# Performance work log

Hardware: AMD Instinct MI355X
Metric: run time of the kernel (lower is better)

Reference implementation:

```python
import jax, jax.numpy as jnp
import numpy as np

NUM_EXPERTS = 8


def setup_inputs() -> dict:
    key = jax.random.key(0)
    k1, k2, k3, k4 = jax.random.split(key, 4)
    T, H, I, E = 1024, 1024, 4096, NUM_EXPERTS
    return {
        "hidden_states": jax.random.normal(k1, (T, H), dtype=jnp.float32),
        "w1": jax.random.normal(k2, (E, 2 * I, H), dtype=jnp.float32) * 0.02,
        "w2": jax.random.normal(k3, (E, H, I), dtype=jnp.float32) * 0.02,
        "gating_output": jax.random.normal(k4, (T, E), dtype=jnp.float32),
        "topk": 2,
    }


def reference(hidden_states, w1, w2, gating_output, topk):
    # Faithful single-device version of jax_fused_moe_func (renormalize=True,
    # reduce_results=True). The original sorts token copies by expert id and runs
    # a grouped matmul (megablox gmm), then reverts the sort; mathematically each
    # token copy is multiplied by its expert's weights, which we compute directly
    # (no sort/unsort permutation needed since it cancels).
    orig_shape = hidden_states.shape
    dtype = hidden_states.dtype
    H = hidden_states.shape[-1]
    T = hidden_states.size // H
    E = w1.shape[0]
    I = w2.shape[-1]  # intermediate_size

    hs = hidden_states.reshape(T, H)
    gates = gating_output.reshape(T, E)

    probs = jax.nn.softmax(gates.astype(jnp.float32), axis=-1)
    topk_weights, topk_indices = jax.lax.top_k(probs, k=topk)
    topk_weights = topk_weights / topk_weights.sum(axis=-1, keepdims=True)  # renormalize
    topk_weights = topk_weights.astype(dtype)

    flat_ids = topk_indices.reshape(-1)            # [T*topk] expert id per token copy
    x = jnp.repeat(hs, topk, axis=0)               # [T*topk, H] token copies

    out = jnp.zeros((T * topk, H), dtype=dtype)
    for e in range(E):  # fixed small expert loop (emulates grouped GEMM)
        h = x @ w1[e].T                            # [m, 2I]
        act = jax.nn.silu(h[:, :I]) * h[:, I:]     # SwiGLU
        y = act @ w2[e].T                          # [m, H]
        out = jnp.where((flat_ids == e)[:, None], y, out)

    out = (out.reshape(T, topk, H) * topk_weights[..., None]).sum(axis=-2)
    return out.reshape(orig_shape)
```

## Files before the change

kernel.cpp:

```cpp
#include <hip/hip_runtime.h>

#define T_TOK 1024
#define H_DIM 1024
#define I_DIM 4096
#define NE 8

typedef __attribute__((ext_vector_type(8))) short bf16x8;
typedef __attribute__((ext_vector_type(4))) float f32x4;
typedef __attribute__((ext_vector_type(8))) unsigned short us8;

__device__ __forceinline__ unsigned short f2bf(float x) {
  union { float f; unsigned u; } v; v.f = x;
  unsigned r = v.u + 0x7fffu + ((v.u >> 16) & 1u);
  return (unsigned short)(r >> 16);
}

__device__ __forceinline__ unsigned cvt_pk_bf16(float a, float b) {
  unsigned r;
  asm("v_cvt_pk_bf16_f32 %0, %1, %2" : "=v"(r) : "v"(a), "v"(b));
  return r;
}

__device__ __forceinline__ void sync_lds() {
  asm volatile("s_waitcnt lgkmcnt(0)" ::: "memory");
  __builtin_amdgcn_s_barrier();
}

__global__ void k_route(const float* __restrict__ gates, int* __restrict__ counts,
                        int* __restrict__ tok_idx, float* __restrict__ tok_w,
                        int* __restrict__ tok_cpy) {
  int t = blockIdx.x * blockDim.x + threadIdx.x;
  if (t >= T_TOK) return;
  float g[NE];
#pragma unroll
  for (int e = 0; e < NE; ++e) g[e] = gates[t * NE + e];
  int i1 = 0; float g1 = g[0];
#pragma unroll
  for (int e = 1; e < NE; ++e) if (g[e] > g1) { g1 = g[e]; i1 = e; }
  int i2 = -1; float g2 = -1e30f;
#pragma unroll
  for (int e = 0; e < NE; ++e) if (e != i1 && g[e] > g2) { g2 = g[e]; i2 = e; }
  float wa = 1.0f / (1.0f + expf(g2 - g1));
  float wb = 1.0f - wa;
  int s1 = atomicAdd(&counts[i1], 1);
  tok_idx[i1 * T_TOK + s1] = t; tok_w[i1 * T_TOK + s1] = wa; tok_cpy[i1 * T_TOK + s1] = 0;
  int s2 = atomicAdd(&counts[i2], 1);
  tok_idx[i2 * T_TOK + s2] = t; tok_w[i2 * T_TOK + s2] = wb; tok_cpy[i2 * T_TOK + s2] = 1;
}

__global__ void k_pack(const float* __restrict__ hs, const int* __restrict__ counts,
                       const int* __restrict__ tok_idx, const float* __restrict__ tok_w,
                       const int* __restrict__ tok_cpy, unsigned short* __restrict__ xpack,
                       float* __restrict__ row_w, int* __restrict__ inv_row) {
  int e = blockIdx.x >> 10, slot = blockIdx.x & 1023;
  if (slot >= counts[e]) return;
  int off = 0;
#pragma unroll
  for (int i = 0; i < NE; ++i) if (i < e) off += counts[i];
  int row = off + slot;
  int tok = tok_idx[e * T_TOK + slot];
  if (threadIdx.x == 0) {
    row_w[row] = tok_w[e * T_TOK + slot];
    inv_row[tok * 2 + tok_cpy[e * T_TOK + slot]] = row;
  }
  float4 v = ((const float4*)(hs + (size_t)tok * H_DIM))[threadIdx.x];
  uint2 o; o.x = cvt_pk_bf16(v.x, v.y); o.y = cvt_pk_bf16(v.z, v.w);
  ((uint2*)(xpack + (size_t)row * H_DIM))[threadIdx.x] = o;
}

#define BK 64

__global__ __launch_bounds__(256)
void k_gemm1(const float* __restrict__ w1, const unsigned short* __restrict__ xpack,
             const int* __restrict__ counts, unsigned short* __restrict__ act) {
  int b = blockIdx.x;
  int panel = b & 1023;
  int mt = b >> 10;
  int e = panel >> 7, ntile = panel & 127;
  int cnt = counts[e];
  int m0 = mt * 128;
  if (m0 >= cnt) return;
  int off = 0;
#pragma unroll
  for (int i = 0; i < NE; ++i) if (i < e) off += counts[i];
  int n0 = ntile * 32;

  __shared__ __align__(16) short As[2][128 * BK];
  __shared__ __align__(16) short Bs[2][64 * BK];

  int tid = threadIdx.x;
  int lane = tid & 63, wid = tid >> 6;
  int wm = wid & 1, wn = wid >> 1;
  int lr = lane & 15, lk8 = (lane >> 4) * 8;

  const float* w1e = w1 + (size_t)e * (2 * I_DIM) * H_DIM;
  const unsigned short* xb = xpack + (size_t)(off + m0) * H_DIM;

  int arow0 = tid >> 3, ack = tid & 7;
  int brow0 = tid >> 4, bck = tid & 15;

  const unsigned short* aptr[4];
  int awoff[4];
#pragma unroll
  for (int i = 0; i < 4; ++i) {
    int r = arow0 + i * 32;
    aptr[i] = xb + (size_t)r * H_DIM + ack * 8;
    awoff[i] = r * BK + ((ack * 8) ^ ((r & 7) << 3));
  }
  const float* bptr[4];
  int bwoff[4];
#pragma unroll
  for (int i = 0; i < 4; ++i) {
    int r = brow0 + i * 16;
    int grow = ((r & 16) ? I_DIM : 0) + n0 + ((r >> 5) << 4) + (r & 15);
    bptr[i] = w1e + (size_t)grow * H_DIM + bck * 4;
    bwoff[i] = r * BK + ((bck * 4) ^ ((r & 7) << 3));
  }

  f32x4 acc[4][2];
#pragma unroll
  for (int i = 0; i < 4; ++i)
#pragma unroll
    for (int j = 0; j < 2; ++j) acc[i][j] = (f32x4){0.f, 0.f, 0.f, 0.f};

  us8 aReg[2][4];
  float4 bReg[2][4];

#define G1_LOAD(SET, KSTEP)                                                     \
  {                                                                             \
    int kq = (KSTEP)*BK;                                                        \
    _Pragma("unroll") for (int i = 0; i < 4; ++i) {                             \
      us8 z = {0, 0, 0, 0, 0, 0, 0, 0};                                         \
      aReg[SET][i] = (m0 + arow0 + i * 32 < cnt) ? *(const us8*)(aptr[i] + kq) : z; \
    }                                                                           \
    _Pragma("unroll") for (int i = 0; i < 4; ++i)                               \
        bReg[SET][i] = *(const float4*)(bptr[i] + kq);                          \
  }

#define G1_STEP(BUF, SET, NEXTK)                                                \
  {                                                                             \
    _Pragma("unroll") for (int i = 0; i < 4; ++i)                               \
        *(us8*)&As[BUF][awoff[i]] = aReg[SET][i];                               \
    _Pragma("unroll") for (int i = 0; i < 4; ++i) {                             \
      float4 v = bReg[SET][i];                                                  \
      uint2 o; o.x = cvt_pk_bf16(v.x, v.y); o.y = cvt_pk_bf16(v.z, v.w);        \
      *(uint2*)&Bs[BUF][bwoff[i]] = o;                                          \
    }                                                                           \
    if ((NEXTK) < H_DIM / BK) G1_LOAD(SET, NEXTK);                              \
    sync_lds();                                                                 \
    _Pragma("unroll") for (int kk = 0; kk < 2; ++kk) {                          \
      int k0 = kk * 32 + lk8;                                                   \
      bf16x8 a[4], bb[2];                                                       \
      _Pragma("unroll") for (int mr = 0; mr < 4; ++mr) {                        \
        int r = wm * 64 + mr * 16 + lr;                                         \
        a[mr] = *(const bf16x8*)&As[BUF][r * BK + (k0 ^ ((r & 7) << 3))];       \
      }                                                                         \
      _Pragma("unroll") for (int nr = 0; nr < 2; ++nr) {                        \
        int r = (wn * 2 + nr) * 16 + lr;                                        \
        bb[nr] = *(const bf16x8*)&Bs[BUF][r * BK + (k0 ^ ((r & 7) << 3))];      \
      }                                                                         \
      _Pragma("unroll") for (int mr = 0; mr < 4; ++mr)                          \
          _Pragma("unroll") for (int nr = 0; nr < 2; ++nr)                      \
              acc[mr][nr] = __builtin_amdgcn_mfma_f32_16x16x32_bf16(            \
                  a[mr], bb[nr], acc[mr][nr], 0, 0, 0);                         \
    }                                                                           \
  }

  G1_LOAD(0, 0);
  G1_LOAD(1, 1);
  for (int ks = 0; ks < H_DIM / BK; ks += 2) {
    G1_STEP(0, 0, ks + 2);
    G1_STEP(1, 1, ks + 3);
  }
#undef G1_LOAD
#undef G1_STEP

#pragma unroll
  for (int mr = 0; mr < 4; ++mr) {
    f32x4 g = acc[mr][0], u = acc[mr][1];
    int ncol = n0 + wn * 16 + lr;
#pragma unroll
    for (int q = 0; q < 4; ++q) {
      int rl = wm * 64 + mr * 16 + (lane >> 4) * 4 + q;
      if (m0 + rl < cnt) {
        float gv = g[q];
        float av = gv / (1.0f + expf(-gv)) * u[q];
        act[(size_t)(off + m0 + rl) * I_DIM + ncol] = f2bf(av);
      }
    }
  }
}

__global__ __launch_bounds__(256)
void k_gemm2(const float* __restrict__ w2, const unsigned short* __restrict__ act,
             const int* __restrict__ counts, const float* __restrict__ row_w,
             float* __restrict__ yp) {
  int b = blockIdx.x;
  int panel = b & 511;
  int mt = b >> 9;
  int e = panel >> 6;
  int nt = (panel & 63) >> 2, kc = panel & 3;
  int cnt = counts[e];
  int m0 = mt * 64;
  if (m0 >= cnt) return;
  int off = 0;
#pragma unroll
  for (int i = 0; i < NE; ++i) if (i < e) off += counts[i];
  int n0 = nt * 64;
  int kbase = kc * 1024;

  __shared__ __align__(16) short As[2][64 * BK];
  __shared__ __align__(16) short Bs[2][64 * BK];

  int tid = threadIdx.x;
  int lane = tid & 63, wid = tid >> 6;
  int wm = wid & 1, wn = wid >> 1;
  int lr = lane & 15, lk8 = (lane >> 4) * 8;

  const float* w2e = w2 + (size_t)e * H_DIM * I_DIM;
  const unsigned short* ab = act + (size_t)(off + m0) * I_DIM;

  int arow0 = tid >> 3, ack = tid & 7;
  int brow0 = tid >> 4, bck = tid & 15;

  const unsigned short* aptr[2];
  int awoff[2];
#pragma unroll
  for (int i = 0; i < 2; ++i) {
    int r = arow0 + i * 32;
    aptr[i] = ab + (size_t)r * I_DIM + kbase + ack * 8;
    awoff[i] = r * BK + ((ack * 8) ^ ((r & 7) << 3));
  }
  const float* bptr[4];
  int bwoff[4];
#pragma unroll
  for (int i = 0; i < 4; ++i) {
    int r = brow0 + i * 16;
    bptr[i] = w2e + (size_t)(n0 + r) * I_DIM + kbase + bck * 4;
    bwoff[i] = r * BK + ((bck * 4) ^ ((r & 7) << 3));
  }

  f32x4 acc[2][2];
#pragma unroll
  for (int i = 0; i < 2; ++i)
#pragma unroll
    for (int j = 0; j < 2; ++j) acc[i][j] = (f32x4){0.f, 0.f, 0.f, 0.f};

  us8 aReg[2][2];
  float4 bReg[2][4];

#define G2_LOAD(SET, KSTEP)                                                     \
  {                                                                             \
    int kq = (KSTEP)*BK;                                                        \
    _Pragma("unroll") for (int i = 0; i < 2; ++i) {                             \
      us8 z = {0, 0, 0, 0, 0, 0, 0, 0};                                         \
      aReg[SET][i] = (m0 + arow0 + i * 32 < cnt) ? *(const us8*)(aptr[i] + kq) : z; \
    }                                                                           \
    _Pragma("unroll") for (int i = 0; i < 4; ++i)                               \
        bReg[SET][i] = *(const float4*)(bptr[i] + kq);                          \
  }

#define G2_STEP(BUF, SET, NEXTK)                                                \
  {                                                                             \
    _Pragma("unroll") for (int i = 0; i < 2; ++i)                               \
        *(us8*)&As[BUF][awoff[i]] = aReg[SET][i];                               \
    _Pragma("unroll") for (int i = 0; i < 4; ++i) {                             \
      float4 v = bReg[SET][i];                                                  \
      uint2 o; o.x = cvt_pk_bf16(v.x, v.y); o.y = cvt_pk_bf16(v.z, v.w);        \
      *(uint2*)&Bs[BUF][bwoff[i]] = o;                                          \
    }                                                                           \
    if ((NEXTK) < 16) G2_LOAD(SET, NEXTK);                                      \
    sync_lds();                                                                 \
    _Pragma("unroll") for (int kk = 0; kk < 2; ++kk) {                          \
      int k0 = kk * 32 + lk8;                                                   \
      bf16x8 a[2], bb[2];                                                       \
      _Pragma("unroll") for (int mr = 0; mr < 2; ++mr) {                        \
        int r = wm * 32 + mr * 16 + lr;                                         \
        a[mr] = *(const bf16x8*)&As[BUF][r * BK + (k0 ^ ((r & 7) << 3))];       \
      }                                                                         \
      _Pragma("unroll") for (int nr = 0; nr < 2; ++nr) {                        \
        int r = wn * 32 + nr * 16 + lr;                                         \
        bb[nr] = *(const bf16x8*)&Bs[BUF][r * BK + (k0 ^ ((r & 7) << 3))];      \
      }                                                                         \
      _Pragma("unroll") for (int mr = 0; mr < 2; ++mr)                          \
          _Pragma("unroll") for (int nr = 0; nr < 2; ++nr)                      \
              acc[mr][nr] = __builtin_amdgcn_mfma_f32_16x16x32_bf16(            \
                  a[mr], bb[nr], acc[mr][nr], 0, 0, 0);                         \
    }                                                                           \
  }

  G2_LOAD(0, 0);
  G2_LOAD(1, 1);
  for (int ks = 0; ks < 16; ks += 2) {
    G2_STEP(0, 0, ks + 2);
    G2_STEP(1, 1, ks + 3);
  }
#undef G2_LOAD
#undef G2_STEP

  float* ypc = yp + (size_t)kc * (2048 * H_DIM);
#pragma unroll
  for (int mr = 0; mr < 2; ++mr) {
#pragma unroll
    for (int q = 0; q < 4; ++q) {
      int rl = wm * 32 + mr * 16 + (lane >> 4) * 4 + q;
      if (m0 + rl >= cnt) continue;
      int grow = off + m0 + rl;
      float wgt = row_w[grow];
      float* yrow = ypc + (size_t)grow * H_DIM;
#pragma unroll
      for (int nr = 0; nr < 2; ++nr) {
        int ncol = n0 + wn * 32 + nr * 16 + lr;
        yrow[ncol] = acc[mr][nr][q] * wgt;
      }
    }
  }
}

__global__ void k_combine(const float* __restrict__ yp, const int* __restrict__ inv_row,
                          float* __restrict__ out) {
  int t = blockIdx.x, i = threadIdx.x;
  int r0 = inv_row[2 * t], r1 = inv_row[2 * t + 1];
  float4 s = make_float4(0.f, 0.f, 0.f, 0.f);
#pragma unroll
  for (int kc = 0; kc < 4; ++kc) {
    const float4* a = (const float4*)(yp + (size_t)kc * (2048 * H_DIM) + (size_t)r0 * H_DIM);
    const float4* b = (const float4*)(yp + (size_t)kc * (2048 * H_DIM) + (size_t)r1 * H_DIM);
    float4 va = a[i], vb = b[i];
    s.x += va.x + vb.x; s.y += va.y + vb.y; s.z += va.z + vb.z; s.w += va.w + vb.w;
  }
  ((float4*)(out + (size_t)t * H_DIM))[i] = s;
}

extern "C" void kernel_launch(void* const* d_in, const int* in_sizes, int n_in,
                              void* d_out, int out_size, void* d_ws, size_t ws_size,
                              hipStream_t stream) {
  const float* hs = (const float*)d_in[0];
  const float* w1 = (const float*)d_in[1];
  const float* w2 = (const float*)d_in[2];
  const float* gates = (const float*)d_in[3];
  float* out = (float*)d_out;

  char* ws = (char*)d_ws;
  int* counts = (int*)ws;
  int* tok_idx = (int*)(ws + 4096);
  float* tok_w = (float*)(ws + 4096 + 32768);
  int* tok_cpy = (int*)(ws + 4096 + 65536);
  float* row_w = (float*)(ws + 4096 + 98304);
  int* inv_row = (int*)(ws + 4096 + 98304 + 8192);
  unsigned short* xpack = (unsigned short*)(ws + (1 << 17));
  unsigned short* act = (unsigned short*)(ws + (8u << 20));
  float* yp = (float*)(ws + (32u << 20));

  hipMemsetAsync(counts, 0, NE * sizeof(int), stream);
  k_route<<<dim3(4), dim3(256), 0, stream>>>(gates, counts, tok_idx, tok_w, tok_cpy);
  k_pack<<<dim3(NE * T_TOK), dim3(256), 0, stream>>>(hs, counts, tok_idx, tok_w, tok_cpy,
                                                     xpack, row_w, inv_row);
  k_gemm1<<<dim3(8192), dim3(256), 0, stream>>>(w1, xpack, counts, act);
  k_gemm2<<<dim3(8192), dim3(256), 0, stream>>>(w2, act, counts, row_w, yp);
  k_combine<<<dim3(T_TOK), dim3(256), 0, stream>>>(yp, inv_row, out);
}
```

Baseline: 245.0 us.

## Use direct global-to-LDS loads with larger tiles and expert-interleaved block order in MoE GEMMs

Both expert GEMMs now stage operands through global_load_lds DMA straight into swizzled LDS buffers, replacing register staging, and convert the fp32 weights to bf16 after reading them from LDS. Tiles grow to 128x64 for gemm1 and 128x128 for gemm2, and the block index is remapped so consecutive blocks cycle across experts. The aim is to cut VGPR traffic and load-issue overhead and to increase operand reuse per block. In exchange, LDS per block roughly doubles because fp32 weights are stored there, which may reduce occupancy, and the conversion work is repeated across waves.

```diff
diff --git a/kernel.cpp b/kernel.cpp
--- a/kernel.cpp
+++ b/kernel.cpp
@@ -4,10 +4,10 @@
 #define H_DIM 1024
 #define I_DIM 4096
 #define NE 8
+#define BK 64
 
 typedef __attribute__((ext_vector_type(8))) short bf16x8;
 typedef __attribute__((ext_vector_type(4))) float f32x4;
-typedef __attribute__((ext_vector_type(8))) unsigned short us8;
 
 __device__ __forceinline__ unsigned short f2bf(float x) {
   union { float f; unsigned u; } v; v.f = x;
@@ -21,10 +21,14 @@
   return r;
 }
 
-__device__ __forceinline__ void sync_lds() {
-  asm volatile("s_waitcnt lgkmcnt(0)" ::: "memory");
-  __builtin_amdgcn_s_barrier();
-}
+__device__ __forceinline__ void dma16(const void* g, void* l) {
+  __builtin_amdgcn_global_load_lds(
+      (const __attribute__((address_space(1))) unsigned*)g,
+      (__attribute__((address_space(3))) unsigned*)l, 16, 0, 0);
+}
+
+#define WAITVM(N) asm volatile("s_waitcnt vmcnt(" #N ")" ::: "memory")
+#define WAITLGKM() asm volatile("s_waitcnt lgkmcnt(0)" ::: "memory")
 
 __global__ void k_route(const float* __restrict__ gates, int* __restrict__ counts,
                         int* __restrict__ tok_idx, float* __restrict__ tok_w,
@@ -68,124 +72,108 @@
   ((uint2*)(xpack + (size_t)row * H_DIM))[threadIdx.x] = o;
 }
 
-#define BK 64
-
 __global__ __launch_bounds__(256)
 void k_gemm1(const float* __restrict__ w1, const unsigned short* __restrict__ xpack,
              const int* __restrict__ counts, unsigned short* __restrict__ act) {
   int b = blockIdx.x;
-  int panel = b & 1023;
-  int mt = b >> 10;
-  int e = panel >> 7, ntile = panel & 127;
+  int x = b & 7;
+  int i = b >> 3;
+  int pe = i >> 3;
+  int mt = i & 7;
+  int e = x, nt = pe;
   int cnt = counts[e];
   int m0 = mt * 128;
   if (m0 >= cnt) return;
   int off = 0;
 #pragma unroll
-  for (int i = 0; i < NE; ++i) if (i < e) off += counts[i];
-  int n0 = ntile * 32;
-
-  __shared__ __align__(16) short As[2][128 * BK];
-  __shared__ __align__(16) short Bs[2][64 * BK];
+  for (int k = 0; k < NE; ++k) if (k < e) off += counts[k];
+  int n0 = nt * 64;
+
+  __shared__ __align__(16) unsigned char AsB[2][16384];
+  __shared__ __align__(16) unsigned char BsB[2][32768];
 
   int tid = threadIdx.x;
   int lane = tid & 63, wid = tid >> 6;
   int wm = wid & 1, wn = wid >> 1;
-  int lr = lane & 15, lk8 = (lane >> 4) * 8;
+  int lr = lane & 15, lg = lane >> 4;
 
   const float* w1e = w1 + (size_t)e * (2 * I_DIM) * H_DIM;
   const unsigned short* xb = xpack + (size_t)(off + m0) * H_DIM;
 
-  int arow0 = tid >> 3, ack = tid & 7;
-  int brow0 = tid >> 4, bck = tid & 15;
-
-  const unsigned short* aptr[4];
-  int awoff[4];
-#pragma unroll
-  for (int i = 0; i < 4; ++i) {
-    int r = arow0 + i * 32;
-    aptr[i] = xb + (size_t)r * H_DIM + ack * 8;
-    awoff[i] = r * BK + ((ack * 8) ^ ((r & 7) << 3));
-  }
-  const float* bptr[4];
-  int bwoff[4];
-#pragma unroll
-  for (int i = 0; i < 4; ++i) {
-    int r = brow0 + i * 16;
-    int grow = ((r & 16) ? I_DIM : 0) + n0 + ((r >> 5) << 4) + (r & 15);
-    bptr[i] = w1e + (size_t)grow * H_DIM + bck * 4;
-    bwoff[i] = r * BK + ((bck * 4) ^ ((r & 7) << 3));
-  }
-
-  f32x4 acc[4][2];
-#pragma unroll
-  for (int i = 0; i < 4; ++i)
-#pragma unroll
-    for (int j = 0; j < 2; ++j) acc[i][j] = (f32x4){0.f, 0.f, 0.f, 0.f};
-
-  us8 aReg[2][4];
-  float4 bReg[2][4];
-
-#define G1_LOAD(SET, KSTEP)                                                     \
+  int arow = tid >> 3, acc8 = tid & 7;
+  const unsigned short* aS0 = xb + (size_t)arow * H_DIM + (size_t)((acc8 ^ (arow & 7)) * 8);
+  int brow = tid >> 4, bcc = tid & 15;
+  int bccs = bcc ^ (brow & 7);
+
+  f32x4 acc[4][4];
+#pragma unroll
+  for (int p = 0; p < 4; ++p)
+#pragma unroll
+    for (int q = 0; q < 4; ++q) acc[p][q] = (f32x4){0.f, 0.f, 0.f, 0.f};
+
+#define G1_STAGE(BUF, T)                                                        \
   {                                                                             \
-    int kq = (KSTEP)*BK;                                                        \
-    _Pragma("unroll") for (int i = 0; i < 4; ++i) {                             \
-      us8 z = {0, 0, 0, 0, 0, 0, 0, 0};                                         \
-      aReg[SET][i] = (m0 + arow0 + i * 32 < cnt) ? *(const us8*)(aptr[i] + kq) : z; \
-    }                                                                           \
-    _Pragma("unroll") for (int i = 0; i < 4; ++i)                               \
-        bReg[SET][i] = *(const float4*)(bptr[i] + kq);                          \
-  }
-
-#define G1_STEP(BUF, SET, NEXTK)                                                \
-  {                                                                             \
-    _Pragma("unroll") for (int i = 0; i < 4; ++i)                               \
-        *(us8*)&As[BUF][awoff[i]] = aReg[SET][i];                               \
-    _Pragma("unroll") for (int i = 0; i < 4; ++i) {                             \
-      float4 v = bReg[SET][i];                                                  \
-      uint2 o; o.x = cvt_pk_bf16(v.x, v.y); o.y = cvt_pk_bf16(v.z, v.w);        \
-      *(uint2*)&Bs[BUF][bwoff[i]] = o;                                          \
-    }                                                                           \
-    if ((NEXTK) < H_DIM / BK) G1_LOAD(SET, NEXTK);                              \
-    sync_lds();                                                                 \
-    _Pragma("unroll") for (int kk = 0; kk < 2; ++kk) {                          \
-      int k0 = kk * 32 + lk8;                                                   \
-      bf16x8 a[4], bb[2];                                                       \
-      _Pragma("unroll") for (int mr = 0; mr < 4; ++mr) {                        \
-        int r = wm * 64 + mr * 16 + lr;                                         \
-        a[mr] = *(const bf16x8*)&As[BUF][r * BK + (k0 ^ ((r & 7) << 3))];       \
-      }                                                                         \
-      _Pragma("unroll") for (int nr = 0; nr < 2; ++nr) {                        \
-        int r = (wn * 2 + nr) * 16 + lr;                                        \
-        bb[nr] = *(const bf16x8*)&Bs[BUF][r * BK + (k0 ^ ((r & 7) << 3))];      \
-      }                                                                         \
+    int k0 = (T) * BK;                                                          \
+    unsigned char* aD = &AsB[BUF][tid * 16];                                    \
+    _Pragma("unroll") for (int c = 0; c < 4; ++c)                               \
+        dma16(aS0 + (size_t)c * 32 * H_DIM + k0, aD + c * 4096);                \
+    unsigned char* bD = &BsB[BUF][tid * 16];                                    \
+    _Pragma("unroll") for (int c = 0; c < 8; ++c) {                             \
+      int grow = ((c & 1) ? I_DIM : 0) + n0 + ((c >> 1) << 4) + brow;           \
+      dma16(w1e + (size_t)grow * H_DIM + bccs * 4 + k0, bD + c * 4096);         \
+    }                                                                           \
+  }
+
+#define G1_COMPUTE(BUF)                                                         \
+  _Pragma("unroll") for (int kk = 0; kk < 2; ++kk) {                            \
+    bf16x8 a[4];                                                                \
+    _Pragma("unroll") for (int mr = 0; mr < 4; ++mr) {                          \
+      int r = wm * 64 + mr * 16 + lr;                                           \
+      int ca = kk * 4 + lg;                                                     \
+      a[mr] = *(const bf16x8*)&AsB[BUF][r * 128 + ((ca ^ (r & 7)) << 4)];       \
+    }                                                                           \
+    _Pragma("unroll") for (int nr = 0; nr < 4; ++nr) {                          \
+      int r = wn * 64 + nr * 16 + lr;                                           \
+      int c0 = kk * 8 + lg * 2;                                                 \
+      f32x4 lo = *(const f32x4*)&BsB[BUF][r * 256 + ((c0 ^ (r & 7)) << 4)];     \
+      f32x4 hi = *(const f32x4*)&BsB[BUF][r * 256 + (((c0 + 1) ^ (r & 7)) << 4)]; \
+      union { unsigned u[4]; bf16x8 v; } bb;                                    \
+      bb.u[0] = cvt_pk_bf16(lo[0], lo[1]); bb.u[1] = cvt_pk_bf16(lo[2], lo[3]); \
+      bb.u[2] = cvt_pk_bf16(hi[0], hi[1]); bb.u[3] = cvt_pk_bf16(hi[2], hi[3]); \
       _Pragma("unroll") for (int mr = 0; mr < 4; ++mr)                          \
-          _Pragma("unroll") for (int nr = 0; nr < 2; ++nr)                      \
-              acc[mr][nr] = __builtin_amdgcn_mfma_f32_16x16x32_bf16(            \
-                  a[mr], bb[nr], acc[mr][nr], 0, 0, 0);                         \
-    }                                                                           \
-  }
-
-  G1_LOAD(0, 0);
-  G1_LOAD(1, 1);
-  for (int ks = 0; ks < H_DIM / BK; ks += 2) {
-    G1_STEP(0, 0, ks + 2);
-    G1_STEP(1, 1, ks + 3);
-  }
-#undef G1_LOAD
-#undef G1_STEP
+          acc[mr][nr] = __builtin_amdgcn_mfma_f32_16x16x32_bf16(                \
+              a[mr], bb.v, acc[mr][nr], 0, 0, 0);                               \
+    }                                                                           \
+  }
+
+  G1_STAGE(0, 0);
+  G1_STAGE(1, 1);
+  for (int t = 0; t < 16; ++t) {
+    if (t == 15) { WAITVM(0); } else { WAITVM(12); }
+    __builtin_amdgcn_s_barrier();
+    __builtin_amdgcn_sched_barrier(0);
+    if (t & 1) { G1_COMPUTE(1); } else { G1_COMPUTE(0); }
+    WAITLGKM();
+    __builtin_amdgcn_s_barrier();
+    if (t + 2 < 16) { if (t & 1) G1_STAGE(1, t + 2) else G1_STAGE(0, t + 2) }
+  }
+#undef G1_STAGE
+#undef G1_COMPUTE
 
 #pragma unroll
   for (int mr = 0; mr < 4; ++mr) {
-    f32x4 g = acc[mr][0], u = acc[mr][1];
-    int ncol = n0 + wn * 16 + lr;
-#pragma unroll
-    for (int q = 0; q < 4; ++q) {
-      int rl = wm * 64 + mr * 16 + (lane >> 4) * 4 + q;
-      if (m0 + rl < cnt) {
-        float gv = g[q];
-        float av = gv / (1.0f + expf(-gv)) * u[q];
-        act[(size_t)(off + m0 + rl) * I_DIM + ncol] = f2bf(av);
+#pragma unroll
+    for (int pp = 0; pp < 2; ++pp) {
+      f32x4 g = acc[mr][2 * pp], u = acc[mr][2 * pp + 1];
+      int ncol = n0 + (wn * 2 + pp) * 16 + lr;
+#pragma unroll
+      for (int q = 0; q < 4; ++q) {
+        int rl = wm * 64 + mr * 16 + lg * 4 + q;
+        if (m0 + rl < cnt) {
+          float gv = g[q];
+          float av = gv / (1.0f + expf(-gv)) * u[q];
+          act[(size_t)(off + m0 + rl) * I_DIM + ncol] = f2bf(av);
+        }
       }
     }
   }
@@ -196,121 +184,104 @@
              const int* __restrict__ counts, const float* __restrict__ row_w,
              float* __restrict__ yp) {
   int b = blockIdx.x;
-  int panel = b & 511;
-  int mt = b >> 9;
-  int e = panel >> 6;
-  int nt = (panel & 63) >> 2, kc = panel & 3;
+  int x = b & 7;
+  int i = b >> 3;
+  int pc = i >> 3;
+  int mt = i & 7;
+  int e = x, nt = pc >> 2, kc = pc & 3;
   int cnt = counts[e];
-  int m0 = mt * 64;
+  int m0 = mt * 128;
   if (m0 >= cnt) return;
   int off = 0;
 #pragma unroll
-  for (int i = 0; i < NE; ++i) if (i < e) off += counts[i];
-  int n0 = nt * 64;
+  for (int k = 0; k < NE; ++k) if (k < e) off += counts[k];
+  int n0 = nt * 128;
   int kbase = kc * 1024;
 
-  __shared__ __align__(16) short As[2][64 * BK];
-  __shared__ __align__(16) short Bs[2][64 * BK];
+  __shared__ __align__(16) unsigned char AsB[2][16384];
+  __shared__ __align__(16) unsigned char BsB[2][32768];
 
   int tid = threadIdx.x;
   int lane = tid & 63, wid = tid >> 6;
   int wm = wid & 1, wn = wid >> 1;
-  int lr = lane & 15, lk8 = (lane >> 4) * 8;
+  int lr = lane & 15, lg = lane >> 4;
 
   const float* w2e = w2 + (size_t)e * H_DIM * I_DIM;
-  const unsigned short* ab = act + (size_t)(off + m0) * I_DIM;
-
-  int arow0 = tid >> 3, ack = tid & 7;
-  int brow0 = tid >> 4, bck = tid & 15;
-
-  const unsigned short* aptr[2];
-  int awoff[2];
-#pragma unroll
-  for (int i = 0; i < 2; ++i) {
-    int r = arow0 + i * 32;
-    aptr[i] = ab + (size_t)r * I_DIM + kbase + ack * 8;
-    awoff[i] = r * BK + ((ack * 8) ^ ((r & 7) << 3));
-  }
-  const float* bptr[4];
-  int bwoff[4];
-#pragma unroll
-  for (int i = 0; i < 4; ++i) {
-    int r = brow0 + i * 16;
-    bptr[i] = w2e + (size_t)(n0 + r) * I_DIM + kbase + bck * 4;
-    bwoff[i] = r * BK + ((bck * 4) ^ ((r & 7) << 3));
-  }
-
-  f32x4 acc[2][2];
-#pragma unroll
-  for (int i = 0; i < 2; ++i)
-#pragma unroll
-    for (int j = 0; j < 2; ++j) acc[i][j] = (f32x4){0.f, 0.f, 0.f, 0.f};
-
-  us8 aReg[2][2];
-  float4 bReg[2][4];
-
-#define G2_LOAD(SET, KSTEP)                                                     \
+  const unsigned short* ab = act + (size_t)(off + m0) * I_DIM + kbase;
+
+  int arow = tid >> 3, acc8 = tid & 7;
+  const unsigned short* aS0 = ab + (size_t)arow * I_DIM + (size_t)((acc8 ^ (arow & 7)) * 8);
+  int brow = tid >> 4, bcc = tid & 15;
+  int bccs = bcc ^ (brow & 7);
+
+  f32x4 acc[4][4];
+#pragma unroll
+  for (int p = 0; p < 4; ++p)
+#pragma unroll
+    for (int q = 0; q < 4; ++q) acc[p][q] = (f32x4){0.f, 0.f, 0.f, 0.f};
+
+#define G2_STAGE(BUF, T)                                                        \
   {                                                                             \
-    int kq = (KSTEP)*BK;                                                        \
-    _Pragma("unroll") for (int i = 0; i < 2; ++i) {                             \
-      us8 z = {0, 0, 0, 0, 0, 0, 0, 0};                                         \
-      aReg[SET][i] = (m0 + arow0 + i * 32 < cnt) ? *(const us8*)(aptr[i] + kq) : z; \
-    }                                                                           \
-    _Pragma("unroll") for (int i = 0; i < 4; ++i)                               \
-        bReg[SET][i] = *(const float4*)(bptr[i] + kq);                          \
-  }
-
-#define G2_STEP(BUF, SET, NEXTK)                                                \
-  {                                                                             \
-    _Pragma("unroll") for (int i = 0; i < 2; ++i)                               \
-        *(us8*)&As[BUF][awoff[i]] = aReg[SET][i];                               \
-    _Pragma("unroll") for (int i = 0; i < 4; ++i) {                             \
-      float4 v = bReg[SET][i];                                                  \
-      uint2 o; o.x = cvt_pk_bf16(v.x, v.y); o.y = cvt_pk_bf16(v.z, v.w);        \
-      *(uint2*)&Bs[BUF][bwoff[i]] = o;                                          \
-    }                                                                           \
-    if ((NEXTK) < 16) G2_LOAD(SET, NEXTK);                                      \
-    sync_lds();                                                                 \
-    _Pragma("unroll") for (int kk = 0; kk < 2; ++kk) {                          \
-      int k0 = kk * 32 + lk8;                                                   \
-      bf16x8 a[2], bb[2];                                                       \
-      _Pragma("unroll") for (int mr = 0; mr < 2; ++mr) {                        \
-        int r = wm * 32 + mr * 16 + lr;                                         \
-        a[mr] = *(const bf16x8*)&As[BUF][r * BK + (k0 ^ ((r & 7) << 3))];       \
-      }                                                                         \
-      _Pragma("unroll") for (int nr = 0; nr < 2; ++nr) {                        \
-        int r = wn * 32 + nr * 16 + lr;                                         \
-        bb[nr] = *(const bf16x8*)&Bs[BUF][r * BK + (k0 ^ ((r & 7) << 3))];      \
-      }                                                                         \
-      _Pragma("unroll") for (int mr = 0; mr < 2; ++mr)                          \
-          _Pragma("unroll") for (int nr = 0; nr < 2; ++nr)                      \
-              acc[mr][nr] = __builtin_amdgcn_mfma_f32_16x16x32_bf16(            \
-                  a[mr], bb[nr], acc[mr][nr], 0, 0, 0);                         \
-    }                                                                           \
-  }
-
-  G2_LOAD(0, 0);
-  G2_LOAD(1, 1);
-  for (int ks = 0; ks < 16; ks += 2) {
-    G2_STEP(0, 0, ks + 2);
-    G2_STEP(1, 1, ks + 3);
-  }
-#undef G2_LOAD
-#undef G2_STEP
+    int k0 = (T) * BK;                                                          \
+    unsigned char* aD = &AsB[BUF][tid * 16];                                    \
+    _Pragma("unroll") for (int c = 0; c < 4; ++c)                               \
+        dma16(aS0 + (size_t)c * 32 * I_DIM + k0, aD + c * 4096);                \
+    unsigned char* bD = &BsB[BUF][tid * 16];                                    \
+    _Pragma("unroll") for (int c = 0; c < 8; ++c) {                             \
+      int grow = n0 + c * 16 + brow;                                            \
+      dma16(w2e + (size_t)grow * I_DIM + kbase + bccs * 4 + k0, bD + c * 4096); \
+    }                                                                           \
+  }
+
+#define G2_COMPUTE(BUF)                                                         \
+  _Pragma("unroll") for (int kk = 0; kk < 2; ++kk) {                            \
+    bf16x8 a[4];                                                                \
+    _Pragma("unroll") for (int mr = 0; mr < 4; ++mr) {                          \
+      int r = wm * 64 + mr * 16 + lr;                                           \
+      int ca = kk * 4 + lg;                                                     \
+      a[mr] = *(const bf16x8*)&AsB[BUF][r * 128 + ((ca ^ (r & 7)) << 4)];       \
+    }                                                                           \
+    _Pragma("unroll") for (int nr = 0; nr < 4; ++nr) {                          \
+      int r = wn * 64 + nr * 16 + lr;                                           \
+      int c0 = kk * 8 + lg * 2;                                                 \
+      f32x4 lo = *(const f32x4*)&BsB[BUF][r * 256 + ((c0 ^ (r & 7)) << 4)];     \
+      f32x4 hi = *(const f32x4*)&BsB[BUF][r * 256 + (((c0 + 1) ^ (r & 7)) << 4)]; \
+      union { unsigned u[4]; bf16x8 v; } bb;                                    \
+      bb.u[0] = cvt_pk_bf16(lo[0], lo[1]); bb.u[1] = cvt_pk_bf16(lo[2], lo[3]); \
+      bb.u[2] = cvt_pk_bf16(hi[0], hi[1]); bb.u[3] = cvt_pk_bf16(hi[2], hi[3]); \
+      _Pragma("unroll") for (int mr = 0; mr < 4; ++mr)                          \
+          acc[mr][nr] = __builtin_amdgcn_mfma_f32_16x16x32_bf16(                \
+              a[mr], bb.v, acc[mr][nr], 0, 0, 0);                               \
+    }                                                                           \
+  }
+
+  G2_STAGE(0, 0);
+  G2_STAGE(1, 1);
+  for (int t = 0; t < 16; ++t) {
+    if (t == 15) { WAITVM(0); } else { WAITVM(12); }
+    __builtin_amdgcn_s_barrier();
+    __builtin_amdgcn_sched_barrier(0);
+    if (t & 1) { G2_COMPUTE(1); } else { G2_COMPUTE(0); }
+    WAITLGKM();
+    __builtin_amdgcn_s_barrier();
+    if (t + 2 < 16) { if (t & 1) G2_STAGE(1, t + 2) else G2_STAGE(0, t + 2) }
+  }
+#undef G2_STAGE
+#undef G2_COMPUTE
 
   float* ypc = yp + (size_t)kc * (2048 * H_DIM);
 #pragma unroll
-  for (int mr = 0; mr < 2; ++mr) {
+  for (int mr = 0; mr < 4; ++mr) {
 #pragma unroll
     for (int q = 0; q < 4; ++q) {
-      int rl = wm * 32 + mr * 16 + (lane >> 4) * 4 + q;
+      int rl = wm * 64 + mr * 16 + lg * 4 + q;
       if (m0 + rl >= cnt) continue;
       int grow = off + m0 + rl;
       float wgt = row_w[grow];
       float* yrow = ypc + (size_t)grow * H_DIM;
 #pragma unroll
-      for (int nr = 0; nr < 2; ++nr) {
-        int ncol = n0 + wn * 32 + nr * 16 + lr;
+      for (int nr = 0; nr < 4; ++nr) {
+        int ncol = n0 + wn * 64 + nr * 16 + lr;
         yrow[ncol] = acc[mr][nr][q] * wgt;
       }
     }
@@ -356,7 +327,7 @@
   k_route<<<dim3(4), dim3(256), 0, stream>>>(gates, counts, tok_idx, tok_w, tok_cpy);
   k_pack<<<dim3(NE * T_TOK), dim3(256), 0, stream>>>(hs, counts, tok_idx, tok_w, tok_cpy,
                                                      xpack, row_w, inv_row);
-  k_gemm1<<<dim3(8192), dim3(256), 0, stream>>>(w1, xpack, counts, act);
-  k_gemm2<<<dim3(8192), dim3(256), 0, stream>>>(w2, act, counts, row_w, yp);
+  k_gemm1<<<dim3(4096), dim3(256), 0, stream>>>(w1, xpack, counts, act);
+  k_gemm2<<<dim3(2048), dim3(256), 0, stream>>>(w2, act, counts, row_w, yp);
   k_combine<<<dim3(T_TOK), dim3(256), 0, stream>>>(yp, inv_row, out);
 }
```

Measured after the change: 349.0 us. 1.42x slower.
